# Performance work log

Measured on AMD Instinct MI355X. Metric: run time of the kernel, lower is better.

Reference implementation:

```python
import jax, jax.numpy as jnp
import numpy as np

NUM_HEADS = 16


def setup_inputs() -> dict:
    key = jax.random.key(0)
    ks = jax.random.split(key, 5)
    B, S, D = 2, 2048, 1024
    scale = 0.02
    return {
        "x": jax.random.normal(ks[0], (B, S, D), dtype=jnp.float32),
        "Wq": jax.random.normal(ks[1], (D, D), dtype=jnp.float32) * scale,
        "Wk": jax.random.normal(ks[2], (D, D), dtype=jnp.float32) * scale,
        "Wv": jax.random.normal(ks[3], (D, D), dtype=jnp.float32) * scale,
        "Wo": jax.random.normal(ks[4], (D, D), dtype=jnp.float32) * scale,
        "bo": jnp.zeros((D,), dtype=jnp.float32),
    }


def reference(x, Wq, Wk, Wv, Wo, bo):
    B, S, D = x.shape
    H = NUM_HEADS
    Dh = D // H
    # project and split heads -> [B, H, S, Dh]
    q = (x @ Wq).reshape(B, S, H, Dh).transpose(0, 2, 1, 3)
    k = (x @ Wk).reshape(B, S, H, Dh).transpose(0, 2, 1, 3)
    v = (x @ Wv).reshape(B, S, H, Dh).transpose(0, 2, 1, 3)
    # full causal attention scores [B, H, S, S]
    scores = jnp.einsum("bhqd,bhkd->bhqk", q, k)
    causal_mask = jnp.triu(jnp.ones((S, S), dtype=bool), k=1)
    scores = jnp.where(causal_mask, -jnp.inf, scores)
    attn = jax.nn.softmax(scores / jnp.sqrt(jnp.float32(Dh)), axis=-1)
    ctx = jnp.einsum("bhqk,bhkd->bhqd", attn, v)
    ctx = ctx.transpose(0, 2, 1, 3).reshape(B, S, D)
    return ctx @ Wo + bo
```

## Files before the change

### kernel.cpp

```cpp
#include <hip/hip_runtime.h>
#include <hip/hip_bf16.h>
#include <math.h>

typedef __bf16 bf16_t;
typedef bf16_t bf16x4 __attribute__((ext_vector_type(4)));
typedef bf16_t bf16x8 __attribute__((ext_vector_type(8)));
typedef float f32x4 __attribute__((ext_vector_type(4)));
typedef unsigned int u32;
typedef u32 u32x2 __attribute__((ext_vector_type(2)));
typedef u32 u32x4 __attribute__((ext_vector_type(4)));

#define MFMA16(a, b, c) __builtin_amdgcn_mfma_f32_16x16x32_bf16(a, b, c, 0, 0, 0)
#define NEG_BIG (-1e30f)
#define QSCALE 0.18033688f

#define GLL16(gp, lp)                                                          \
    __builtin_amdgcn_global_load_lds(                                          \
        (const __attribute__((address_space(1))) unsigned int*)(gp),           \
        (__attribute__((address_space(3))) unsigned int*)(lp), 16, 0, 0)


__global__ __launch_bounds__(256) void prep(const float* __restrict__ x,
                                            const float* __restrict__ Wq,
                                            const float* __restrict__ Wk,
                                            const float* __restrict__ Wv,
                                            const float* __restrict__ Wo,
                                            bf16_t* __restrict__ Xb,
                                            bf16_t* __restrict__ WTqkv,
                                            bf16_t* __restrict__ WoT) {
    __shared__ float tile[32][33];
    const int z = blockIdx.z;
    const int tx = threadIdx.x, ty = threadIdx.y;
    if (z == 4) {
        int i0 = (((blockIdx.y * 32 + blockIdx.x) * 256) + ty * 32 + tx) * 4;
        for (int j = 0; j < 4; j++) {
            int i = i0 + j * 1048576;
            float4 v = *(const float4*)(x + i);
            Xb[i + 0] = (bf16_t)v.x;
            Xb[i + 1] = (bf16_t)v.y;
            Xb[i + 2] = (bf16_t)v.z;
            Xb[i + 3] = (bf16_t)v.w;
        }
    } else {
        const float* W = (z == 0) ? Wq : (z == 1) ? Wk : (z == 2) ? Wv : Wo;
        bf16_t* WT = (z < 3) ? (WTqkv + (size_t)z * 1048576) : WoT;
        int bx = blockIdx.x * 32, by = blockIdx.y * 32;
        for (int i = 0; i < 32; i += 8)
            tile[ty + i][tx] = W[(size_t)(by + ty + i) * 1024 + bx + tx];
        __syncthreads();
        for (int i = 0; i < 32; i += 8)
            WT[(size_t)(bx + ty + i) * 1024 + by + tx] = (bf16_t)tile[tx][ty + i];
    }
}

__global__ __launch_bounds__(256) void gemm_qkv(const bf16_t* __restrict__ X,
                                                const bf16_t* __restrict__ WT,
                                                bf16_t* __restrict__ Qd,
                                                bf16_t* __restrict__ Kd,
                                                bf16_t* __restrict__ Vd) {
    __shared__ bf16_t AsmF[128 * 64];
    __shared__ bf16_t BsmF[128 * 64];
    const int which = blockIdx.z;
    const bf16_t* Wt = WT + (size_t)which * 1024 * 1024;
    const int bm = blockIdx.y * 128;
    const int bn = blockIdx.x * 128;
    const int tid = threadIdx.x;
    const int wave = tid >> 6, lane = tid & 63;
    const int wm = (wave >> 1) * 64, wn = (wave & 1) * 64;
    const int col = lane & 15, quad = lane >> 4;
    const int cswz = col & 7;
    const int lr8 = lane >> 3;
    const int jg = (lane & 7) ^ lr8;

    const int srow = wave * 32 + lr8;
    const bf16_t* gA = X  + (size_t)(bm + srow) * 1024 + jg * 8;
    const bf16_t* gB = Wt + (size_t)(bn + srow) * 1024 + jg * 8;
    bf16_t* lA = AsmF + wave * 2048;
    bf16_t* lB = BsmF + wave * 2048;

    f32x4 acc[4][4] = {};

    for (int k0 = 0; k0 < 1024; k0 += 64) {
        for (int j = 0; j < 4; j++) {
            GLL16(gA + (size_t)j * 8192 + k0, lA + j * 512);
            GLL16(gB + (size_t)j * 8192 + k0, lB + j * 512);
        }
        __syncthreads();
        for (int ks = 0; ks < 2; ks++) {
            bf16x8 af[4], bfr[4];
            for (int mi = 0; mi < 4; mi++)
                af[mi] = *(const bf16x8*)&AsmF[(wm + mi * 16 + col) * 64 +
                                               (((ks << 2) + quad) ^ cswz) * 8];
            for (int ni = 0; ni < 4; ni++)
                bfr[ni] = *(const bf16x8*)&BsmF[(wn + ni * 16 + col) * 64 +
                                                (((ks << 2) + quad) ^ cswz) * 8];
            if (which != 2) {
                for (int mi = 0; mi < 4; mi++)
                    for (int ni = 0; ni < 4; ni++)
                        acc[mi][ni] = MFMA16(af[mi], bfr[ni], acc[mi][ni]);
            } else {
                for (int mi = 0; mi < 4; mi++)
                    for (int ni = 0; ni < 4; ni++)
                        acc[mi][ni] = MFMA16(bfr[ni], af[mi], acc[mi][ni]);
            }
        }
        __syncthreads();
    }

    if (which != 2) {
        const float sc = (which == 0) ? QSCALE : 1.0f;
        for (int mi = 0; mi < 4; mi++) {
            for (int ni = 0; ni < 4; ni++) {
                int mbase = bm + wm + mi * 16 + quad * 4;
                int n = bn + wn + ni * 16 + col;
                int h = n >> 6, dh = n & 63;
                for (int r = 0; r < 4; r++) {
                    int m = mbase + r;
                    int b = m >> 11, s = m & 2047;
                    size_t bh = (size_t)b * 16 + h;
                    bf16_t val = (bf16_t)(acc[mi][ni][r] * sc);
                    if (which == 0) Qd[(bh * 2048 + s) * 64 + dh] = val;
                    else            Kd[(bh * 2048 + s) * 64 + dh] = val;
                }
            }
        }
    } else {
        for (int mi = 0; mi < 4; mi++) {
            for (int ni = 0; ni < 4; ni++) {
                int nbase = bn + wn + ni * 16 + quad * 4;
                int m = bm + wm + mi * 16 + col;
                int b = m >> 11, s = m & 2047;
                for (int r = 0; r < 4; r++) {
                    int n = nbase + r;
                    int h = n >> 6, dh = n & 63;
                    size_t bh = (size_t)b * 16 + h;
                    Vd[(bh * 64 + dh) * 2048 + s] = (bf16_t)acc[mi][ni][r];
                }
            }
        }
    }
}

__global__ __launch_bounds__(256) void attn(const bf16_t* __restrict__ Q,
                                            const bf16_t* __restrict__ K,
                                            const bf16_t* __restrict__ VT,
                                            bf16_t* __restrict__ CTX) {
    __shared__ bf16_t KsF[2 * 64 * 64];
    __shared__ bf16_t VsF[2 * 64 * 64];

    const int bidx = blockIdx.x;
    const int bh = bidx & 31;
    const int qt = 31 - (bidx >> 5);
    const int tid = threadIdx.x;
    const int wave = tid >> 6, lane = tid & 63;
    const int col = lane & 15, quad = lane >> 4;
    const int cswz = col & 7;
    const int lr8 = lane >> 3;
    const int jg = (lane & 7) ^ lr8;

    const bf16_t* Qb = Q + (size_t)bh * 2048 * 64;
    const bf16_t* Kb = K + (size_t)bh * 2048 * 64;
    const bf16_t* Vb = VT + (size_t)bh * 64 * 2048;

    const int strow = wave * 16 + lr8;
    const bf16_t* gK = Kb + (size_t)strow * 64 + jg * 8;
    const bf16_t* gV = Vb + (size_t)strow * 2048 + jg * 8;

    const int b_ = bh >> 4, h_ = bh & 15;

    bf16x8 ones;
    for (int i = 0; i < 8; i++) ones[i] = (bf16_t)1.0f;

    auto stage = [&](int k0, int bsel) {
        bf16_t* lK = KsF + bsel * 4096 + wave * 1024;
        bf16_t* lV = VsF + bsel * 4096 + wave * 1024;
        for (int j = 0; j < 2; j++) {
            GLL16(gK + (size_t)(k0 + j * 8) * 64, lK + j * 512);
            GLL16(gV + (size_t)(k0 + j * 8 * 2048), lV + j * 512);
        }
    };

    stage(0, 0);

    const int q0 = qt * 64;
    const int qrow = q0 + wave * 16 + col;
    const bf16x8 qf0 = *(const bf16x8*)&Qb[(size_t)qrow * 64 + quad * 8];
    const bf16x8 qf1 = *(const bf16x8*)&Qb[(size_t)qrow * 64 + 32 + quad * 8];

    f32x4 o[4] = {};
    f32x4 accl = {};

    const int iA = (col | ((quad & 1) << 5)) << 2;
    const bool hi = (quad & 2) != 0;

    const int nt = qt + 1;
    for (int g = 0; g < nt; g++) {
        __syncthreads();
        if (g + 1 < nt) stage((g + 1) * 64, (g + 1) & 1);

        const int bsel = g & 1;
        const bf16_t* Kbuf = KsF + bsel * 4096;
        const bf16_t* Vbuf = VsF + bsel * 4096;
        const bool diag = (g == qt);

        u32x2 pwd[4];
#pragma unroll
        for (int ksub = 0; ksub < 4; ksub++) {
            bf16x8 a0 = *(const bf16x8*)&Kbuf[(ksub * 16 + col) * 64 +
                                              (quad ^ cswz) * 8];
            bf16x8 a1 = *(const bf16x8*)&Kbuf[(ksub * 16 + col) * 64 +
                                              ((4 + quad) ^ cswz) * 8];
            f32x4 z = {};
            z = MFMA16(a0, qf0, z);
            z = MFMA16(a1, qf1, z);
            if (diag) {
                for (int r = 0; r < 4; r++) {
                    int lk = ksub * 16 + quad * 4 + r;
                    if (lk > wave * 16 + col) z[r] = NEG_BIG;
                }
            }
            bf16x4 pw;
#pragma unroll
            for (int r = 0; r < 4; r++)
                pw[r] = (bf16_t)__builtin_amdgcn_exp2f(z[r]);
            pwd[ksub] = __builtin_bit_cast(u32x2, pw);
        }

#pragma unroll
        for (int ck = 0; ck < 2; ck++) {
            u32x2 sA = pwd[2 * ck], sB = pwd[2 * ck + 1];
            int w0a = __builtin_amdgcn_ds_bpermute(iA,      (int)sA.x);
            int w0b = __builtin_amdgcn_ds_bpermute(iA,      (int)sB.x);
            int w1a = __builtin_amdgcn_ds_bpermute(iA,      (int)sA.y);
            int w1b = __builtin_amdgcn_ds_bpermute(iA,      (int)sB.y);
            int w2a = __builtin_amdgcn_ds_bpermute(iA + 64, (int)sA.x);
            int w2b = __builtin_amdgcn_ds_bpermute(iA + 64, (int)sB.x);
            int w3a = __builtin_amdgcn_ds_bpermute(iA + 64, (int)sA.y);
            int w3b = __builtin_amdgcn_ds_bpermute(iA + 64, (int)sB.y);
            u32x4 pu = {(u32)(hi ? w0b : w0a), (u32)(hi ? w1b : w1a),
                        (u32)(hi ? w2b : w2a), (u32)(hi ? w3b : w3a)};
            bf16x8 pf = __builtin_bit_cast(bf16x8, pu);

            accl = MFMA16(pf, ones, accl);
            for (int d = 0; d < 4; d++) {
                bf16x8 vf = *(const bf16x8*)&Vbuf[(d * 16 + col) * 64 +
                                                  (((ck << 2) + quad) ^ cswz) * 8];
                o[d] = MFMA16(pf, vf, o[d]);
            }
        }
    }

    for (int r = 0; r < 4; r++) {
        float rl = __builtin_amdgcn_rcpf(fmaxf(accl[r], 1e-20f));
        int s = q0 + wave * 16 + quad * 4 + r;
        for (int d = 0; d < 4; d++) {
            CTX[((size_t)(b_ * 2048 + s)) * 1024 + h_ * 64 + d * 16 + col] =
                (bf16_t)(o[d][r] * rl);
        }
    }
}

__global__ __launch_bounds__(256) void gemm_out(const bf16_t* __restrict__ X,
                                                const bf16_t* __restrict__ WT,
                                                const float* __restrict__ BO,
                                                float* __restrict__ OUT) {
    __shared__ bf16_t AsmF[64 * 64];
    __shared__ bf16_t BsmF[128 * 64];
    const int bm = blockIdx.y * 64;
    const int bn = blockIdx.x * 128;
    const int tid = threadIdx.x;
    const int wave = tid >> 6, lane = tid & 63;
    const int wm = (wave >> 1) * 32, wn = (wave & 1) * 64;
    const int col = lane & 15, quad = lane >> 4;
    const int cswz = col & 7;
    const int lr8 = lane >> 3;
    const int jg = (lane & 7) ^ lr8;

    const int arow = wave * 16 + lr8;
    const int brow = wave * 32 + lr8;
    const bf16_t* gA = X  + (size_t)(bm + arow) * 1024 + jg * 8;
    const bf16_t* gB = WT + (size_t)(bn + brow) * 1024 + jg * 8;
    bf16_t* lA = AsmF + wave * 1024;
    bf16_t* lB = BsmF + wave * 2048;

    f32x4 acc[2][4] = {};

    for (int k0 = 0; k0 < 1024; k0 += 64) {
        for (int j = 0; j < 2; j++)
            GLL16(gA + (size_t)j * 8192 + k0, lA + j * 512);
        for (int j = 0; j < 4; j++)
            GLL16(gB + (size_t)j * 8192 + k0, lB + j * 512);
        __syncthreads();
        for (int ks = 0; ks < 2; ks++) {
            bf16x8 af[2], bfr[4];
            for (int mi = 0; mi < 2; mi++)
                af[mi] = *(const bf16x8*)&AsmF[(wm + mi * 16 + col) * 64 +
                                               (((ks << 2) + quad) ^ cswz) * 8];
            for (int ni = 0; ni < 4; ni++)
                bfr[ni] = *(const bf16x8*)&BsmF[(wn + ni * 16 + col) * 64 +
                                                (((ks << 2) + quad) ^ cswz) * 8];
            for (int mi = 0; mi < 2; mi++)
                for (int ni = 0; ni < 4; ni++)
                    acc[mi][ni] = MFMA16(af[mi], bfr[ni], acc[mi][ni]);
        }
        __syncthreads();
    }

    for (int mi = 0; mi < 2; mi++) {
        for (int ni = 0; ni < 4; ni++) {
            int mbase = bm + wm + mi * 16 + quad * 4;
            int n = bn + wn + ni * 16 + col;
            float bov = BO[n];
            for (int r = 0; r < 4; r++) {
                int m = mbase + r;
                OUT[(size_t)m * 1024 + n] = acc[mi][ni][r] + bov;
            }
        }
    }
}

extern "C" void kernel_launch(void* const* d_in, const int* in_sizes, int n_in,
                              void* d_out, int out_size, void* d_ws, size_t ws_size,
                              hipStream_t stream) {
    const float* x  = (const float*)d_in[0];
    const float* Wq = (const float*)d_in[1];
    const float* Wk = (const float*)d_in[2];
    const float* Wv = (const float*)d_in[3];
    const float* Wo = (const float*)d_in[4];
    const float* bo = (const float*)d_in[5];
    float* out = (float*)d_out;

    const size_t MEG = 1048576;
    bf16_t* base  = (bf16_t*)d_ws;
    bf16_t* Xb    = base;
    bf16_t* WTqkv = base + 4 * MEG;
    bf16_t* WoT   = base + 7 * MEG;
    bf16_t* Qb    = base + 8 * MEG;
    bf16_t* Kb    = base + 12 * MEG;
    bf16_t* Vb    = base + 16 * MEG;
    bf16_t* Cb    = base + 20 * MEG;

    prep<<<dim3(32, 32, 5), dim3(32, 8), 0, stream>>>(x, Wq, Wk, Wv, Wo,
                                                      Xb, WTqkv, WoT);
    gemm_qkv<<<dim3(8, 32, 3), 256, 0, stream>>>(Xb, WTqkv, Qb, Kb, Vb);
    attn<<<1024, 256, 0, stream>>>(Qb, Kb, Vb, Cb);
    gemm_out<<<dim3(8, 64), 256, 0, stream>>>(Cb, WoT, bo, out);
}
```

Measured before the change: 180.1 us.

## Double-buffer LDS tiles in GEMMs and remap blocks for XCD locality

```diff
diff --git a/kernel.cpp b/kernel.cpp
--- a/kernel.cpp
+++ b/kernel.cpp
@@ -58,12 +58,15 @@
                                                 bf16_t* __restrict__ Qd,
                                                 bf16_t* __restrict__ Kd,
                                                 bf16_t* __restrict__ Vd) {
-    __shared__ bf16_t AsmF[128 * 64];
-    __shared__ bf16_t BsmF[128 * 64];
-    const int which = blockIdx.z;
+    __shared__ bf16_t AsmF[2][128 * 64];
+    __shared__ bf16_t BsmF[2][128 * 64];
+    const int bid = blockIdx.x;
+    const int logical = (bid & 7) * 96 + (bid >> 3);
+    const int which = logical >> 8;
+    const int rem = logical & 255;
     const bf16_t* Wt = WT + (size_t)which * 1024 * 1024;
-    const int bm = blockIdx.y * 128;
-    const int bn = blockIdx.x * 128;
+    const int bm = (rem >> 3) * 128;
+    const int bn = (rem & 7) * 128;
     const int tid = threadIdx.x;
     const int wave = tid >> 6, lane = tid & 63;
     const int wm = (wave >> 1) * 64, wn = (wave & 1) * 64;
@@ -75,25 +78,33 @@
     const int srow = wave * 32 + lr8;
     const bf16_t* gA = X  + (size_t)(bm + srow) * 1024 + jg * 8;
     const bf16_t* gB = Wt + (size_t)(bn + srow) * 1024 + jg * 8;
-    bf16_t* lA = AsmF + wave * 2048;
-    bf16_t* lB = BsmF + wave * 2048;
-
-    f32x4 acc[4][4] = {};
-
-    for (int k0 = 0; k0 < 1024; k0 += 64) {
+
+    auto stage = [&](int k0, int bsel) {
+        bf16_t* lA = AsmF[bsel] + wave * 2048;
+        bf16_t* lB = BsmF[bsel] + wave * 2048;
         for (int j = 0; j < 4; j++) {
             GLL16(gA + (size_t)j * 8192 + k0, lA + j * 512);
             GLL16(gB + (size_t)j * 8192 + k0, lB + j * 512);
         }
+    };
+
+    stage(0, 0);
+
+    f32x4 acc[4][4] = {};
+
+    for (int t = 0; t < 16; t++) {
         __syncthreads();
+        if (t + 1 < 16) stage((t + 1) * 64, (t + 1) & 1);
+        const bf16_t* Ab = AsmF[t & 1];
+        const bf16_t* Bb = BsmF[t & 1];
         for (int ks = 0; ks < 2; ks++) {
             bf16x8 af[4], bfr[4];
             for (int mi = 0; mi < 4; mi++)
-                af[mi] = *(const bf16x8*)&AsmF[(wm + mi * 16 + col) * 64 +
-                                               (((ks << 2) + quad) ^ cswz) * 8];
+                af[mi] = *(const bf16x8*)&Ab[(wm + mi * 16 + col) * 64 +
+                                             (((ks << 2) + quad) ^ cswz) * 8];
             for (int ni = 0; ni < 4; ni++)
-                bfr[ni] = *(const bf16x8*)&BsmF[(wn + ni * 16 + col) * 64 +
-                                                (((ks << 2) + quad) ^ cswz) * 8];
+                bfr[ni] = *(const bf16x8*)&Bb[(wn + ni * 16 + col) * 64 +
+                                              (((ks << 2) + quad) ^ cswz) * 8];
             if (which != 2) {
                 for (int mi = 0; mi < 4; mi++)
                     for (int ni = 0; ni < 4; ni++)
@@ -104,7 +115,6 @@
                         acc[mi][ni] = MFMA16(bfr[ni], af[mi], acc[mi][ni]);
             }
         }
-        __syncthreads();
     }
 
     if (which != 2) {
@@ -264,10 +274,12 @@
                                                 const bf16_t* __restrict__ WT,
                                                 const float* __restrict__ BO,
                                                 float* __restrict__ OUT) {
-    __shared__ bf16_t AsmF[64 * 64];
-    __shared__ bf16_t BsmF[128 * 64];
-    const int bm = blockIdx.y * 64;
-    const int bn = blockIdx.x * 128;
+    __shared__ bf16_t AsmF[2][64 * 64];
+    __shared__ bf16_t BsmF[2][128 * 64];
+    const int bid = blockIdx.x;
+    const int logical = (bid & 7) * 64 + (bid >> 3);
+    const int bm = (logical >> 3) * 64;
+    const int bn = (logical & 7) * 128;
     const int tid = threadIdx.x;
     const int wave = tid >> 6, lane = tid & 63;
     const int wm = (wave >> 1) * 32, wn = (wave & 1) * 64;
@@ -280,30 +292,37 @@
     const int brow = wave * 32 + lr8;
     const bf16_t* gA = X  + (size_t)(bm + arow) * 1024 + jg * 8;
     const bf16_t* gB = WT + (size_t)(bn + brow) * 1024 + jg * 8;
-    bf16_t* lA = AsmF + wave * 1024;
-    bf16_t* lB = BsmF + wave * 2048;
-
-    f32x4 acc[2][4] = {};
-
-    for (int k0 = 0; k0 < 1024; k0 += 64) {
+
+    auto stage = [&](int k0, int bsel) {
+        bf16_t* lA = AsmF[bsel] + wave * 1024;
+        bf16_t* lB = BsmF[bsel] + wave * 2048;
         for (int j = 0; j < 2; j++)
             GLL16(gA + (size_t)j * 8192 + k0, lA + j * 512);
         for (int j = 0; j < 4; j++)
             GLL16(gB + (size_t)j * 8192 + k0, lB + j * 512);
+    };
+
+    stage(0, 0);
+
+    f32x4 acc[2][4] = {};
+
+    for (int t = 0; t < 16; t++) {
         __syncthreads();
+        if (t + 1 < 16) stage((t + 1) * 64, (t + 1) & 1);
+        const bf16_t* Ab = AsmF[t & 1];
+        const bf16_t* Bb = BsmF[t & 1];
         for (int ks = 0; ks < 2; ks++) {
             bf16x8 af[2], bfr[4];
             for (int mi = 0; mi < 2; mi++)
-                af[mi] = *(const bf16x8*)&AsmF[(wm + mi * 16 + col) * 64 +
-                                               (((ks << 2) + quad) ^ cswz) * 8];
+                af[mi] = *(const bf16x8*)&Ab[(wm + mi * 16 + col) * 64 +
+                                             (((ks << 2) + quad) ^ cswz) * 8];
             for (int ni = 0; ni < 4; ni++)
-                bfr[ni] = *(const bf16x8*)&BsmF[(wn + ni * 16 + col) * 64 +
-                                                (((ks << 2) + quad) ^ cswz) * 8];
+                bfr[ni] = *(const bf16x8*)&Bb[(wn + ni * 16 + col) * 64 +
+                                              (((ks << 2) + quad) ^ cswz) * 8];
             for (int mi = 0; mi < 2; mi++)
                 for (int ni = 0; ni < 4; ni++)
                     acc[mi][ni] = MFMA16(af[mi], bfr[ni], acc[mi][ni]);
         }
-        __syncthreads();
     }
 
     for (int mi = 0; mi < 2; mi++) {
@@ -342,7 +361,7 @@
 
     prep<<<dim3(32, 32, 5), dim3(32, 8), 0, stream>>>(x, Wq, Wk, Wv, Wo,
                                                       Xb, WTqkv, WoT);
-    gemm_qkv<<<dim3(8, 32, 3), 256, 0, stream>>>(Xb, WTqkv, Qb, Kb, Vb);
+    gemm_qkv<<<768, 256, 0, stream>>>(Xb, WTqkv, Qb, Kb, Vb);
     attn<<<1024, 256, 0, stream>>>(Qb, Kb, Vb, Cb);
-    gemm_out<<<dim3(8, 64), 256, 0, stream>>>(Cb, WoT, bo, out);
-}
+    gemm_out<<<512, 256, 0, stream>>>(Cb, WoT, bo, out);
+}
```

New measurement: 183.2 us. About the same (+1.7%).
